# Kernel tuning notes

Hardware: AMD Instinct MI355X
Metric: run time of the kernel (lower is better)

Reference implementation:

```python
import jax, jax.numpy as jnp
import numpy as np
from jax import lax

IN_DIM, HID = 64, 32


def _lstm_dir(x, Wih, Whh, bih, bhh, reverse=False):
    # x: [B, L, HID] -> hs: [B, L, HID]
    B = x.shape[0]
    H = Whh.shape[1]
    xs = jnp.swapaxes(x, 0, 1)  # [L, B, HID]
    if reverse:
        xs = xs[::-1]

    def step(carry, xt):
        h, c = carry
        gates = xt @ Wih.T + h @ Whh.T + bih + bhh  # [B, 4H]
        i, f, g, o = jnp.split(gates, 4, axis=-1)
        i = jax.nn.sigmoid(i)
        f = jax.nn.sigmoid(f)
        g = jnp.tanh(g)
        o = jax.nn.sigmoid(o)
        c = f * c + i * g
        h = o * jnp.tanh(c)
        return (h, c), h

    h0 = jnp.zeros((B, H), x.dtype)
    _, hs = lax.scan(step, (h0, h0), xs)
    if reverse:
        hs = hs[::-1]
    return jnp.swapaxes(hs, 0, 1)


def setup_inputs() -> dict:
    key = jax.random.key(0)
    ks = jax.random.split(key, 20)
    B, L = 32, 16384
    s = 1.0 / np.sqrt(HID)
    u = lambda k, shape: jax.random.uniform(k, shape, jnp.float32, -s, s)
    inp = {
        'features': jax.random.normal(ks[0], (B, IN_DIM, L), jnp.float32),
        'proj_W': u(ks[1], (HID, IN_DIM)), 'proj_b': u(ks[2], (HID,)),
        'Wih_f': u(ks[3], (4 * HID, HID)), 'Whh_f': u(ks[4], (4 * HID, HID)),
        'bih_f': u(ks[5], (4 * HID,)), 'bhh_f': u(ks[6], (4 * HID,)),
        'Wih_b': u(ks[7], (4 * HID, HID)), 'Whh_b': u(ks[8], (4 * HID, HID)),
        'bih_b': u(ks[9], (4 * HID,)), 'bhh_b': u(ks[10], (4 * HID,)),
        'bc_W1': u(ks[11], (HID, 2 * HID)), 'bc_b1': u(ks[12], (HID,)),
        'bc_W2': u(ks[13], (1, HID)), 'bc_b2': u(ks[14], (1,)),
        'rc_W': u(ks[15], (1, 2 * HID)), 'rc_b': u(ks[16], (1,)),
    }
    return inp


def reference(features, proj_W, proj_b, Wih_f, Whh_f, bih_f, bhh_f,
              Wih_b, Whh_b, bih_b, bhh_b, bc_W1, bc_b1, bc_W2, bc_b2,
              rc_W, rc_b):
    # is_sequence=True path: [B, C, L] -> [B, L, C]
    x = jnp.swapaxes(features, 1, 2)
    projected = x @ proj_W.T + proj_b  # [B, L, HID]
    h_f = _lstm_dir(projected, Wih_f, Whh_f, bih_f, bhh_f, reverse=False)
    h_b = _lstm_dir(projected, Wih_b, Whh_b, bih_b, bhh_b, reverse=True)
    lstm_out = jnp.concatenate([h_f, h_b], axis=-1)  # [B, L, 2*HID]

    # boundary classifier applied to every timestep (vectorized)
    h1 = jax.nn.relu(lstm_out @ bc_W1.T + bc_b1)
    probs = jax.nn.sigmoid(h1 @ bc_W2.T + bc_b2)[..., 0]  # [B, L]
    probs = probs.at[:, 0].multiply(1.2).at[:, -1].multiply(1.2)
    probs = jnp.clip(probs, 0.0, 1.0)

    # boundary adjustment (vectorized neighbor comparison)
    left = probs[:, 1:-1] - probs[:, :-2]
    right = probs[:, 1:-1] - probs[:, 2:]
    adj_in = jnp.where((left < 0) & (jnp.abs(left) > jnp.abs(right)), -1.0,
                       jnp.where((right < 0) & (jnp.abs(right) > jnp.abs(left)), 1.0, 0.0))
    zpad = jnp.zeros((probs.shape[0], 1), probs.dtype)
    adj = jnp.concatenate([zpad, adj_in, zpad], axis=1)

    real_prob = jax.nn.sigmoid(lstm_out.mean(axis=1) @ rc_W.T + rc_b)  # [B, 1]
    return probs, adj, real_prob
```

## Files before the change

### kernel.cpp

```cpp
#include <hip/hip_runtime.h>
#include <hip/hip_bf16.h>
#include <stdint.h>

#define LSEQ   16384
#define BATCH  32
#define HIDN   32
#define NGATE  128
#define INDIM  64

typedef float v2f __attribute__((ext_vector_type(2)));
typedef int   v2i __attribute__((ext_vector_type(2)));

__device__ __forceinline__ float fsig(float x) { return 1.f / (1.f + expf(-x)); }

__device__ __forceinline__ float readlane_f(float v, int l) {
    return __uint_as_float((unsigned)__builtin_amdgcn_readlane((int)__float_as_uint(v), l));
}

__device__ __forceinline__ float xswap32(float x) {
    v2i r = __builtin_amdgcn_permlane32_swap(
        (int)__float_as_uint(x), (int)__float_as_uint(x), false, false);
    return __uint_as_float((unsigned)r.y);
}

__global__ __launch_bounds__(256) void k_prep(
    const float* __restrict__ bih_f, const float* __restrict__ bhh_f,
    const float* __restrict__ bih_b, const float* __restrict__ bhh_b,
    float* __restrict__ bias2, double* __restrict__ hsum, float* __restrict__ state)
{
    int gid = blockIdx.x * 256 + threadIdx.x;
    if (gid < 256) {
        int dd = gid >> 7, jj = gid & 127;
        float bi = dd ? bih_b[jj] : bih_f[jj];
        float bh = dd ? bhh_b[jj] : bhh_f[jj];
        bias2[gid] = __fadd_rn(bi, bh);
    }
    if (gid < 2 * BATCH * HIDN) hsum[gid] = 0.0;
    state[gid] = 0.f;
}

__device__ __forceinline__ void gx_device(
    const float* __restrict__ features,
    const float* __restrict__ proj_W,
    const float* __restrict__ proj_b,
    const float* __restrict__ Wih_f,
    const float* __restrict__ Wih_b,
    const float* __restrict__ bias2,
    float* __restrict__ gx,
    int chunkT, int s0, int blk, int tid)
{
    int tilesPerB = chunkT >> 8;
    int b  = blk / tilesPerB;
    int tt = (blk % tilesPerB) * 256 + tid;
    int s  = s0 + tt;

    #pragma unroll 1
    for (int d = 0; d < 2; ++d) {
        int t = d ? (LSEQ - 1 - s) : s;
        float f[INDIM];
        #pragma unroll
        for (int k = 0; k < INDIM; ++k)
            f[k] = features[((size_t)b * INDIM + k) * LSEQ + t];

        float proj[HIDN];
        #pragma unroll 1
        for (int m = 0; m < HIDN; ++m) {
            double sA = 0.0, sB = 0.0, sC = 0.0, sD = 0.0;
            #pragma unroll
            for (int k = 0; k < INDIM; k += 4) {
                sA += (double)proj_W[m * INDIM + k + 0] * (double)f[k + 0];
                sB += (double)proj_W[m * INDIM + k + 1] * (double)f[k + 1];
                sC += (double)proj_W[m * INDIM + k + 2] * (double)f[k + 2];
                sD += (double)proj_W[m * INDIM + k + 3] * (double)f[k + 3];
            }
            proj[m] = (float)(((double)proj_b[m] + sA + sB) + (sC + sD));
        }

        const float* Wih = d ? Wih_b : Wih_f;
        const float* bs  = bias2 + d * NGATE;
        float2* out2 = (float2*)(gx + (((size_t)(d * BATCH + b) * chunkT + tt) << 7));
        #pragma unroll 1
        for (int kq = 0; kq < HIDN; ++kq) {
            const float* Wi = Wih + (kq)      * HIDN;
            const float* Wf = Wih + (kq + 32) * HIDN;
            const float* Wg = Wih + (kq + 64) * HIDN;
            const float* Wo = Wih + (kq + 96) * HIDN;
            double si_e = 0, si_o = 0, sf_e = 0, sf_o = 0;
            double sg_e = 0, sg_o = 0, so_e = 0, so_o = 0;
            #pragma unroll
            for (int m = 0; m < HIDN; m += 2) {
                double pe = (double)proj[m], po = (double)proj[m + 1];
                si_e += (double)Wi[m] * pe;  si_o += (double)Wi[m + 1] * po;
                sf_e += (double)Wf[m] * pe;  sf_o += (double)Wf[m + 1] * po;
                sg_e += (double)Wg[m] * pe;  sg_o += (double)Wg[m + 1] * po;
                so_e += (double)Wo[m] * pe;  so_o += (double)Wo[m + 1] * po;
            }
            float2 vif, vgo;
            vif.x = (float)(((double)bs[kq]      + si_e) + si_o);
            vif.y = (float)(((double)bs[kq + 32] + sf_e) + sf_o);
            vgo.x = (float)(((double)bs[kq + 64] + sg_e) + sg_o);
            vgo.y = (float)(((double)bs[kq + 96] + so_e) + so_o);
            out2[kq]      = vif;
            out2[32 + kq] = vgo;
        }
    }
}

__global__ __launch_bounds__(256) void k_gx(
    const float* __restrict__ features, const float* __restrict__ proj_W,
    const float* __restrict__ proj_b, const float* __restrict__ Wih_f,
    const float* __restrict__ Wih_b, const float* __restrict__ bias2,
    float* __restrict__ gx, int chunkT, int s0)
{
    gx_device(features, proj_W, proj_b, Wih_f, Wih_b, bias2, gx,
              chunkT, s0, blockIdx.x, threadIdx.x);
}

#define LSTM_STEP(CURV, IDX) do {                                             \
    v2f acc = v2f{(CURV).x, (CURV).y};                                        \
    _Pragma("unroll")                                                         \
    for (int m = 0; m < HIDN; ++m) {                                          \
        float hm = readlane_f(hcur, m);                                       \
        acc = __builtin_elementwise_fma(wv[m], v2f{hm, hm}, acc);             \
    }                                                                         \
    float g0 = acc.x, g1 = acc.y;                                             \
    float e0 = __expf(qA * g0);                                               \
    float a0 = numA / (1.f + e0) + addA;                                      \
    float e1 = __expf(-g1);                                                   \
    float a1 = 1.f / (1.f + e1);                                              \
    float xg = xswap32(a0);                                                   \
    float xo = xswap32(a1);                                                   \
    float p1 = __fmul_rn(a1, c_my);                                           \
    float p2 = __fmul_rn(a0, xg);                                             \
    float cn = __fadd_rn(p1, p2);                                             \
    float ec = __expf(-2.f * cn);                                             \
    float tc = 2.f / (1.f + ec) - 1.f;                                        \
    float hn = __fmul_rn(xo, tc);                                             \
    c_my = cn; hcur = hn;                                                     \
    hs_my += (double)hn;                                                      \
    hp[(IDX) * HSTEP * HIDN] = hn;                                            \
} while (0)

template<int HSTEP>
__device__ __forceinline__ void rec_body(
    const float2* __restrict__ gq2, float* __restrict__ hp,
    v2f (&wv)[HIDN], float qA, float numA, float addA,
    float& hcur, float& c_my, double& hs_my,
    int chunkT, int lane)
{
    const ptrdiff_t adv = (lane < HIDN) ? (ptrdiff_t)16 * HSTEP * HIDN : 0;

    float2 A[8], B[8];
    #pragma unroll
    for (int u = 0; u < 8; ++u) A[u] = gq2[u * 64 + lane];

    #pragma unroll 1
    for (int tt = 0; tt < chunkT; tt += 16) {
        #pragma unroll
        for (int u = 0; u < 8; ++u) {
            B[u] = gq2[(u + 8) * 64 + lane];
            LSTM_STEP(A[u], u);
        }
        #pragma unroll
        for (int u = 0; u < 8; ++u) {
            A[u] = gq2[(u + 16) * 64 + lane];
            LSTM_STEP(B[u], 8 + u);
        }
        gq2 += 16 * 64;
        hp  += adv;
    }
}

__global__ __launch_bounds__(256)
__attribute__((amdgpu_waves_per_eu(1)))
void k_fused(
    const float* __restrict__ gxSrc,
    float* __restrict__ gxDst,
    const float* __restrict__ features, const float* __restrict__ proj_W,
    const float* __restrict__ proj_b, const float* __restrict__ Wih_f,
    const float* __restrict__ Wih_b, const float* __restrict__ bias2,
    const float* __restrict__ Whh_f,
    const float* __restrict__ Whh_b,
    float* __restrict__ hbuf,
    float* __restrict__ state,
    double* __restrict__ hsum,
    float* __restrict__ trash,
    int chunkT, int s0_rec, int s0_gx)
{
    if (blockIdx.x >= 64) {
        gx_device(features, proj_W, proj_b, Wih_f, Wih_b, bias2, gxDst,
                  chunkT, s0_gx, blockIdx.x - 64, threadIdx.x);
        return;
    }
    if (threadIdx.x >= 64) return;
    __builtin_amdgcn_s_setprio(1);

    const int wg   = blockIdx.x;
    const int d    = wg >> 5;
    const int lane = threadIdx.x;
    const int k    = lane & 31;
    const int half = lane >> 5;
    const int r0   = k + (half << 6);
    const int r1   = r0 + 32;

    const float qA   = half ? -2.f : -1.f;
    const float numA = half ?  2.f :  1.f;
    const float addA = half ? -1.f :  0.f;

    const float* whh = d ? Whh_b : Whh_f;
    v2f wv[HIDN];
    #pragma unroll
    for (int q = 0; q < 8; ++q) {
        float4 a = *reinterpret_cast<const float4*>(whh + r0 * HIDN + 4 * q);
        float4 b = *reinterpret_cast<const float4*>(whh + r1 * HIDN + 4 * q);
        wv[4 * q + 0] = v2f{a.x, b.x};
        wv[4 * q + 1] = v2f{a.y, b.y};
        wv[4 * q + 2] = v2f{a.z, b.z};
        wv[4 * q + 3] = v2f{a.w, b.w};
    }

    float* st = state + (wg << 6);
    float hcur = st[k];
    float c_my = st[HIDN + k];
    double hs_my = (lane < HIDN) ? hsum[wg * HIDN + lane] : 0.0;

    const float2* gq2 = reinterpret_cast<const float2*>(gxSrc) + ((size_t)wg * chunkT << 6);
    const int t0 = d ? (LSEQ - 1 - s0_rec) : s0_rec;
    float* hpreal = hbuf + (((size_t)wg * LSEQ + t0) << 5) + k;
    float* hp = (lane < HIDN) ? hpreal : (trash + 2048 + lane);

    if (d == 0)
        rec_body<+1>(gq2, hp, wv, qA, numA, addA, hcur, c_my, hs_my, chunkT, lane);
    else
        rec_body<-1>(gq2, hp, wv, qA, numA, addA, hcur, c_my, hs_my, chunkT, lane);

    if (lane < HIDN) {
        st[lane] = hcur;
        st[HIDN + lane] = c_my;
        hsum[wg * HIDN + lane] = hs_my;
    }
}

__global__ __launch_bounds__(256) void k_probs(
    const float* __restrict__ hbuf,
    const float* __restrict__ bcW1, const float* __restrict__ bcb1,
    const float* __restrict__ bcW2, const float* __restrict__ bcb2,
    float* __restrict__ out)
{
    int idx = blockIdx.x * 256 + threadIdx.x;
    int t = idx & (LSEQ - 1);
    int b = idx >> 14;

    float h[64];
    const float* pf = hbuf + (((size_t)b * LSEQ + t) << 5);
    const float* pb = hbuf + (((size_t)(BATCH + b) * LSEQ + t) << 5);
    #pragma unroll
    for (int q = 0; q < 8; ++q) {
        float4 v = reinterpret_cast<const float4*>(pf)[q];
        h[q * 4] = v.x; h[q * 4 + 1] = v.y; h[q * 4 + 2] = v.z; h[q * 4 + 3] = v.w;
    }
    #pragma unroll
    for (int q = 0; q < 8; ++q) {
        float4 v = reinterpret_cast<const float4*>(pb)[q];
        h[32 + q * 4] = v.x; h[32 + q * 4 + 1] = v.y; h[32 + q * 4 + 2] = v.z; h[32 + q * 4 + 3] = v.w;
    }

    double a2 = (double)bcb2[0];
    #pragma unroll 1
    for (int m = 0; m < 32; ++m) {
        double ae = 0.0, ao = 0.0;
        #pragma unroll
        for (int kk = 0; kk < 64; kk += 2) {
            ae += (double)bcW1[m * 64 + kk]     * (double)h[kk];
            ao += (double)bcW1[m * 64 + kk + 1] * (double)h[kk + 1];
        }
        float af = fmaxf((float)(((double)bcb1[m] + ae) + ao), 0.f);
        a2 += (double)bcW2[m] * (double)af;
    }
    float p = fsig((float)a2);
    if (t == 0 || t == LSEQ - 1) p = __fmul_rn(p, 1.2f);
    p = fminf(fmaxf(p, 0.f), 1.f);
    out[idx] = p;
}

__global__ __launch_bounds__(256) void k_adj(
    const float* __restrict__ probs, float* __restrict__ adj)
{
    int idx = blockIdx.x * 256 + threadIdx.x;
    int t = idx & (LSEQ - 1);
    float a = 0.f;
    if (t > 0 && t < LSEQ - 1) {
        float p = probs[idx], pm = probs[idx - 1], pp = probs[idx + 1];
        float left = __fadd_rn(p, -pm), right = __fadd_rn(p, -pp);
        float al = fabsf(left), ar = fabsf(right);
        if (left < 0.f && al > ar)       a = -1.f;
        else if (right < 0.f && ar > al) a =  1.f;
    }
    adj[idx] = a;
}

__global__ __launch_bounds__(64) void k_realp(
    const double* __restrict__ hsum, const float* __restrict__ rcW,
    const float* __restrict__ rcb, float* __restrict__ out)
{
    int b = threadIdx.x;
    if (b < BATCH) {
        const double invL = 1.0 / (double)LSEQ;
        double acc = (double)rcb[0];
        #pragma unroll
        for (int kk = 0; kk < 32; ++kk) {
            acc += hsum[b * 32 + kk] * invL * (double)rcW[kk];
            acc += hsum[(BATCH + b) * 32 + kk] * invL * (double)rcW[32 + kk];
        }
        out[b] = fsig((float)acc);
    }
}

extern "C" void kernel_launch(void* const* d_in, const int* in_sizes, int n_in,
                              void* d_out, int out_size, void* d_ws, size_t ws_size,
                              hipStream_t stream)
{
    (void)in_sizes; (void)n_in; (void)out_size;
    const float* features = (const float*)d_in[0];
    const float* proj_W   = (const float*)d_in[1];
    const float* proj_b   = (const float*)d_in[2];
    const float* Wih_f    = (const float*)d_in[3];
    const float* Whh_f    = (const float*)d_in[4];
    const float* bih_f    = (const float*)d_in[5];
    const float* bhh_f    = (const float*)d_in[6];
    const float* Wih_b    = (const float*)d_in[7];
    const float* Whh_b    = (const float*)d_in[8];
    const float* bih_b    = (const float*)d_in[9];
    const float* bhh_b    = (const float*)d_in[10];
    const float* bcW1     = (const float*)d_in[11];
    const float* bcb1     = (const float*)d_in[12];
    const float* bcW2     = (const float*)d_in[13];
    const float* bcb2     = (const float*)d_in[14];
    const float* rcW      = (const float*)d_in[15];
    const float* rcb      = (const float*)d_in[16];

    char* ws = (char*)d_ws;
    float*  bias2 = (float*)(ws + 65536);
    double* hsum  = (double*)(ws + 66560);
    float*  state = (float*)(ws + 82944);
    float*  trash = (float*)(ws + 102400);
    const size_t HBYTES = (size_t)2 * BATCH * LSEQ * HIDN * sizeof(float);
    float* hbuf = (float*)(ws + (1u << 20));
    const size_t GXOFF = (1u << 20) + HBYTES;

    auto gxstride = [](int c) { return (size_t)c * 32768 + 16384; };
    int chunkT = LSEQ;
    bool dbuf = true;
    while (chunkT > 256 && GXOFF + 2 * gxstride(chunkT) > ws_size) chunkT >>= 1;
    if (GXOFF + 2 * gxstride(chunkT) > ws_size) {
        dbuf = false;
        chunkT = LSEQ;
        while (chunkT > 256 && GXOFF + gxstride(chunkT) > ws_size) chunkT >>= 1;
    }
    const int nch = LSEQ / chunkT;
    float* gx0 = (float*)(ws + GXOFF);
    float* gx1 = dbuf ? (float*)(ws + GXOFF + gxstride(chunkT)) : gx0;

    float* outp = (float*)d_out;
    const int BL = BATCH * LSEQ;
    const int gxblocks = BATCH * (chunkT >> 8);

    k_prep<<<16, 256, 0, stream>>>(bih_f, bhh_f, bih_b, bhh_b, bias2, hsum, state);
    k_gx<<<gxblocks, 256, 0, stream>>>(features, proj_W, proj_b,
                                       Wih_f, Wih_b, bias2, gx0, chunkT, 0);
    for (int c = 0; c < nch; ++c) {
        float* src = (c & 1) ? gx1 : gx0;
        float* dst = (c & 1) ? gx0 : gx1;
        if (dbuf) {
            bool more = (c + 1 < nch);
            k_fused<<<64 + (more ? gxblocks : 0), 256, 0, stream>>>(
                src, dst, features, proj_W, proj_b, Wih_f, Wih_b, bias2,
                Whh_f, Whh_b, hbuf, state, hsum, trash,
                chunkT, c * chunkT, (c + 1) * chunkT);
        } else {
            if (c > 0)
                k_gx<<<gxblocks, 256, 0, stream>>>(features, proj_W, proj_b,
                                                   Wih_f, Wih_b, bias2, gx0,
                                                   chunkT, c * chunkT);
            k_fused<<<64, 256, 0, stream>>>(
                gx0, gx0, features, proj_W, proj_b, Wih_f, Wih_b, bias2,
                Whh_f, Whh_b, hbuf, state, hsum, trash,
                chunkT, c * chunkT, 0);
        }
    }
    k_probs<<<BL / 256, 256, 0, stream>>>(hbuf, bcW1, bcb1, bcW2, bcb2, outp);
    k_adj<<<BL / 256, 256, 0, stream>>>(outp, outp + BL);
    k_realp<<<1, 64, 0, stream>>>(hsum, rcW, rcb, outp + 2 * BL);
}
```

Before: 4.735 ms.

## Interleave two batch recurrences per wavefront to hide serial latency

```diff
diff --git a/kernel.cpp b/kernel.cpp
--- a/kernel.cpp
+++ b/kernel.cpp
@@ -116,58 +116,86 @@
               chunkT, s0, blockIdx.x, threadIdx.x);
 }
 
-#define LSTM_STEP(CURV, IDX) do {                                             \
-    v2f acc = v2f{(CURV).x, (CURV).y};                                        \
-    _Pragma("unroll")                                                         \
-    for (int m = 0; m < HIDN; ++m) {                                          \
-        float hm = readlane_f(hcur, m);                                       \
-        acc = __builtin_elementwise_fma(wv[m], v2f{hm, hm}, acc);             \
-    }                                                                         \
-    float g0 = acc.x, g1 = acc.y;                                             \
-    float e0 = __expf(qA * g0);                                               \
-    float a0 = numA / (1.f + e0) + addA;                                      \
-    float e1 = __expf(-g1);                                                   \
-    float a1 = 1.f / (1.f + e1);                                              \
-    float xg = xswap32(a0);                                                   \
-    float xo = xswap32(a1);                                                   \
-    float p1 = __fmul_rn(a1, c_my);                                           \
-    float p2 = __fmul_rn(a0, xg);                                             \
-    float cn = __fadd_rn(p1, p2);                                             \
-    float ec = __expf(-2.f * cn);                                             \
-    float tc = 2.f / (1.f + ec) - 1.f;                                        \
-    float hn = __fmul_rn(xo, tc);                                             \
-    c_my = cn; hcur = hn;                                                     \
-    hs_my += (double)hn;                                                      \
-    hp[(IDX) * HSTEP * HIDN] = hn;                                            \
-} while (0)
-
 template<int HSTEP>
-__device__ __forceinline__ void rec_body(
-    const float2* __restrict__ gq2, float* __restrict__ hp,
-    v2f (&wv)[HIDN], float qA, float numA, float addA,
-    float& hcur, float& c_my, double& hs_my,
+__device__ __forceinline__ void lstm_step2(
+    float2 cvA, float2 cvB, int idx,
+    v2f (&wv)[HIDN], float qq, float nn, float aa,
+    float& hcurA, float& cA, double& hsA, float* hpA,
+    float& hcurB, float& cB, double& hsB, float* hpB)
+{
+    v2f accA = v2f{cvA.x, cvA.y};
+    v2f accB = v2f{cvB.x, cvB.y};
+    #pragma unroll
+    for (int m = 0; m < HIDN; ++m) {
+        float hmA = readlane_f(hcurA, m);
+        float hmB = readlane_f(hcurB, m);
+        accA = __builtin_elementwise_fma(wv[m], v2f{hmA, hmA}, accA);
+        accB = __builtin_elementwise_fma(wv[m], v2f{hmB, hmB}, accB);
+    }
+    float g0A = accA.x, g1A = accA.y;
+    float g0B = accB.x, g1B = accB.y;
+    float e0A = __expf(qq * g0A);
+    float e0B = __expf(qq * g0B);
+    float a0A = nn / (1.f + e0A) + aa;
+    float a0B = nn / (1.f + e0B) + aa;
+    float e1A = __expf(-g1A);
+    float e1B = __expf(-g1B);
+    float a1A = 1.f / (1.f + e1A);
+    float a1B = 1.f / (1.f + e1B);
+    float xgA = xswap32(a0A);
+    float xgB = xswap32(a0B);
+    float xoA = xswap32(a1A);
+    float xoB = xswap32(a1B);
+    float cnA = __fadd_rn(__fmul_rn(a1A, cA), __fmul_rn(a0A, xgA));
+    float cnB = __fadd_rn(__fmul_rn(a1B, cB), __fmul_rn(a0B, xgB));
+    float ecA = __expf(-2.f * cnA);
+    float ecB = __expf(-2.f * cnB);
+    float tcA = 2.f / (1.f + ecA) - 1.f;
+    float tcB = 2.f / (1.f + ecB) - 1.f;
+    float hnA = __fmul_rn(xoA, tcA);
+    float hnB = __fmul_rn(xoB, tcB);
+    cA = cnA; hcurA = hnA; hsA += (double)hnA;
+    cB = cnB; hcurB = hnB; hsB += (double)hnB;
+    hpA[idx * HSTEP * HIDN] = hnA;
+    hpB[idx * HSTEP * HIDN] = hnB;
+}
+
+template<int HSTEP>
+__device__ __forceinline__ void rec_body2(
+    const float2* __restrict__ gqA, const float2* __restrict__ gqB,
+    float* __restrict__ hpA, float* __restrict__ hpB,
+    v2f (&wv)[HIDN], float qq, float nn, float aa,
+    float& hcurA, float& cA, double& hsA,
+    float& hcurB, float& cB, double& hsB,
     int chunkT, int lane)
 {
     const ptrdiff_t adv = (lane < HIDN) ? (ptrdiff_t)16 * HSTEP * HIDN : 0;
 
-    float2 A[8], B[8];
+    float2 PA[8], QA[8], PB[8], QB[8];
     #pragma unroll
-    for (int u = 0; u < 8; ++u) A[u] = gq2[u * 64 + lane];
+    for (int u = 0; u < 8; ++u) {
+        PA[u] = gqA[u * 64 + lane];
+        PB[u] = gqB[u * 64 + lane];
+    }
 
     #pragma unroll 1
     for (int tt = 0; tt < chunkT; tt += 16) {
         #pragma unroll
         for (int u = 0; u < 8; ++u) {
-            B[u] = gq2[(u + 8) * 64 + lane];
-            LSTM_STEP(A[u], u);
+            QA[u] = gqA[(u + 8) * 64 + lane];
+            QB[u] = gqB[(u + 8) * 64 + lane];
+            lstm_step2<HSTEP>(PA[u], PB[u], u, wv, qq, nn, aa,
+                              hcurA, cA, hsA, hpA, hcurB, cB, hsB, hpB);
         }
         #pragma unroll
         for (int u = 0; u < 8; ++u) {
-            A[u] = gq2[(u + 16) * 64 + lane];
-            LSTM_STEP(B[u], 8 + u);
-        }
-        gq2 += 16 * 64;
-        hp  += adv;
+            PA[u] = gqA[(u + 16) * 64 + lane];
+            PB[u] = gqB[(u + 16) * 64 + lane];
+            lstm_step2<HSTEP>(QA[u], QB[u], 8 + u, wv, qq, nn, aa,
+                              hcurA, cA, hsA, hpA, hcurB, cB, hsB, hpB);
+        }
+        gqA += 16 * 64; gqB += 16 * 64;
+        hpA += adv;     hpB += adv;
     }
 }
 
@@ -187,25 +215,27 @@
     float* __restrict__ trash,
     int chunkT, int s0_rec, int s0_gx)
 {
-    if (blockIdx.x >= 64) {
+    if (blockIdx.x >= 32) {
         gx_device(features, proj_W, proj_b, Wih_f, Wih_b, bias2, gxDst,
-                  chunkT, s0_gx, blockIdx.x - 64, threadIdx.x);
+                  chunkT, s0_gx, blockIdx.x - 32, threadIdx.x);
         return;
     }
     if (threadIdx.x >= 64) return;
     __builtin_amdgcn_s_setprio(1);
 
-    const int wg   = blockIdx.x;
-    const int d    = wg >> 5;
+    const int blk  = blockIdx.x;
+    const int d    = blk >> 4;
+    const int wgA  = d * 32 + (blk & 15);
+    const int wgB  = wgA + 16;
     const int lane = threadIdx.x;
     const int k    = lane & 31;
     const int half = lane >> 5;
     const int r0   = k + (half << 6);
     const int r1   = r0 + 32;
 
-    const float qA   = half ? -2.f : -1.f;
-    const float numA = half ?  2.f :  1.f;
-    const float addA = half ? -1.f :  0.f;
+    const float qq = half ? -2.f : -1.f;
+    const float nn = half ?  2.f :  1.f;
+    const float aa = half ? -1.f :  0.f;
 
     const float* whh = d ? Whh_b : Whh_f;
     v2f wv[HIDN];
@@ -219,25 +249,33 @@
         wv[4 * q + 3] = v2f{a.w, b.w};
     }
 
-    float* st = state + (wg << 6);
-    float hcur = st[k];
-    float c_my = st[HIDN + k];
-    double hs_my = (lane < HIDN) ? hsum[wg * HIDN + lane] : 0.0;
-
-    const float2* gq2 = reinterpret_cast<const float2*>(gxSrc) + ((size_t)wg * chunkT << 6);
+    float* stA = state + (wgA << 6);
+    float* stB = state + (wgB << 6);
+    float hcurA = stA[k],        hcurB = stB[k];
+    float cA    = stA[HIDN + k], cB    = stB[HIDN + k];
+    double hsA = (lane < HIDN) ? hsum[wgA * HIDN + lane] : 0.0;
+    double hsB = (lane < HIDN) ? hsum[wgB * HIDN + lane] : 0.0;
+
+    const float2* gqA = reinterpret_cast<const float2*>(gxSrc) + ((size_t)wgA * chunkT << 6);
+    const float2* gqB = reinterpret_cast<const float2*>(gxSrc) + ((size_t)wgB * chunkT << 6);
     const int t0 = d ? (LSEQ - 1 - s0_rec) : s0_rec;
-    float* hpreal = hbuf + (((size_t)wg * LSEQ + t0) << 5) + k;
-    float* hp = (lane < HIDN) ? hpreal : (trash + 2048 + lane);
+    float* hpAr = hbuf + (((size_t)wgA * LSEQ + t0) << 5) + k;
+    float* hpBr = hbuf + (((size_t)wgB * LSEQ + t0) << 5) + k;
+    float* hpA = (lane < HIDN) ? hpAr : (trash + 1024 + lane);
+    float* hpB = (lane < HIDN) ? hpBr : (trash + 1024 + 128 + lane);
 
     if (d == 0)
-        rec_body<+1>(gq2, hp, wv, qA, numA, addA, hcur, c_my, hs_my, chunkT, lane);
+        rec_body2<+1>(gqA, gqB, hpA, hpB, wv, qq, nn, aa,
+                      hcurA, cA, hsA, hcurB, cB, hsB, chunkT, lane);
     else
-        rec_body<-1>(gq2, hp, wv, qA, numA, addA, hcur, c_my, hs_my, chunkT, lane);
+        rec_body2<-1>(gqA, gqB, hpA, hpB, wv, qq, nn, aa,
+                      hcurA, cA, hsA, hcurB, cB, hsB, chunkT, lane);
 
     if (lane < HIDN) {
-        st[lane] = hcur;
-        st[HIDN + lane] = c_my;
-        hsum[wg * HIDN + lane] = hs_my;
+        stA[lane] = hcurA;        stB[lane] = hcurB;
+        stA[HIDN + lane] = cA;    stB[HIDN + lane] = cB;
+        hsum[wgA * HIDN + lane] = hsA;
+        hsum[wgB * HIDN + lane] = hsB;
     }
 }
 
@@ -373,7 +411,7 @@
         float* dst = (c & 1) ? gx0 : gx1;
         if (dbuf) {
             bool more = (c + 1 < nch);
-            k_fused<<<64 + (more ? gxblocks : 0), 256, 0, stream>>>(
+            k_fused<<<32 + (more ? gxblocks : 0), 256, 0, stream>>>(
                 src, dst, features, proj_W, proj_b, Wih_f, Wih_b, bias2,
                 Whh_f, Whh_b, hbuf, state, hsum, trash,
                 chunkT, c * chunkT, (c + 1) * chunkT);
@@ -382,7 +420,7 @@
                 k_gx<<<gxblocks, 256, 0, stream>>>(features, proj_W, proj_b,
                                                    Wih_f, Wih_b, bias2, gx0,
                                                    chunkT, c * chunkT);
-            k_fused<<<64, 256, 0, stream>>>(
+            k_fused<<<32, 256, 0, stream>>>(
                 gx0, gx0, features, proj_W, proj_b, Wih_f, Wih_b, bias2,
                 Whh_f, Whh_b, hbuf, state, hsum, trash,
                 chunkT, c * chunkT, 0);
```

New measurement: 8.567 ms. +80.9%, slower.
